# Kernel optimization log

Hardware: AMD Instinct MI355X
Metric: run time of the kernel (lower is better)

The kernel has to match this reference:

```python
import math
import jax, jax.numpy as jnp
import numpy as np

B, T, E = 16, 4096, 512


def setup_inputs() -> dict:
    key = jax.random.key(0)
    kq, kk, kv = jax.random.split(key, 3)
    Q = jax.random.normal(kq, (B, T, E), dtype=jnp.float32)
    K = jax.random.normal(kk, (B, T, E), dtype=jnp.float32)
    V = jax.random.normal(kv, (B, T, E), dtype=jnp.float32)
    return {"Q": Q, "K": K, "V": V}


def reference(Q, K, V):
    b, t, e = V.shape
    # --- FFT autocorrelation: replacement for QK^T ---
    qf = jnp.fft.rfft(Q, axis=1)
    kf = jnp.fft.rfft(K, axis=1)
    attn = jnp.fft.irfft(qf * jnp.conj(kf), n=t, axis=1)  # [B, T, E]

    # --- time-delay aggregation (autocorrelation_factor = 2) ---
    top_k = int(2 * math.log(t))                 # 16 for T=4096
    mean_corr = attn.mean(axis=-1)               # mean over heads(=1) & channel -> [B, T]
    global_mean = mean_corr.mean(axis=0)         # batch-shared delay scores [T]
    _, delays = jax.lax.top_k(global_mean, top_k)  # [top_k] int delays
    w = jax.nn.softmax(mean_corr[:, delays], axis=-1)  # per-batch weights [B, top_k]

    t_idx = jnp.arange(t)

    def body(acc, dw):
        d, wk = dw                               # scalar delay, [B] weights
        rolled = V[:, (t_idx + d) % t, :]        # roll(shifts=-d, dims=1) via modular gather
        return acc + rolled * wk[:, None, None], None

    out, _ = jax.lax.scan(body, jnp.zeros_like(V), (delays, w.T))
    return out
```

## Files before the change

### kernel.cpp

```cpp
#include <hip/hip_runtime.h>
#include <math.h>

#define TB 16
#define TT 4096
#define TE 512
#define NF 2049
#define TOPK 16

__device__ __forceinline__ int dr4(int u) {
  return ((u & 3) << 10) | (((u >> 2) & 3) << 8) | (((u >> 4) & 3) << 6) |
         (((u >> 6) & 3) << 4) | (((u >> 8) & 3) << 2) | ((u >> 10) & 3);
}
__device__ __forceinline__ int swz(int i) { return i ^ (i >> 4); }
__device__ __forceinline__ float2 cmul(float2 a, float2 b) {
  return make_float2(a.x * b.x - a.y * b.y, a.x * b.y + a.y * b.x);
}

extern "C" __global__ void __launch_bounds__(512)
k1_spec(const float* __restrict__ Qg, const float* __restrict__ Kg, float* __restrict__ S) {
  __shared__ float2 z[4][4096];
  __shared__ float2 tw[1024];
  const int tid = threadIdx.x;
  const int b   = blockIdx.x >> 4;
  const int grp = blockIdx.x & 15;

  for (int k = tid; k < 1024; k += 512) {
    float s, c;
    sincosf(-6.283185307179586f * (float)k / 4096.0f, &s, &c);
    tw[k] = make_float2(c, s);
  }

  float accr[5] = {0, 0, 0, 0, 0};
  float acci[5] = {0, 0, 0, 0, 0};
  const size_t base = (size_t)b * TT * TE;
  const int ch = tid >> 7;
  const int l  = tid & 127;

  for (int it = 0; it < 8; ++it) {
    const int e0 = grp * 32 + it * 4;
    __syncthreads();
    for (int j = 0; j < 8; ++j) {
      const int t = tid + 512 * j;
      const float4 q4 = *(const float4*)(Qg + base + (size_t)t * TE + e0);
      const float4 k4 = *(const float4*)(Kg + base + (size_t)t * TE + e0);
      const int p = swz(t);
      z[0][p] = make_float2(q4.x, k4.x);
      z[1][p] = make_float2(q4.y, k4.y);
      z[2][p] = make_float2(q4.z, k4.z);
      z[3][p] = make_float2(q4.w, k4.w);
    }
    __syncthreads();

    float2* zz = z[ch];
#pragma unroll
    for (int s = 0; s < 6; ++s) {
      const int M  = 4096 >> (2 * s);
      const int Qq = M >> 2;
      const int LQ = 10 - 2 * s;
      for (int q = 0; q < 8; ++q) {
        const int v    = l + 128 * q;
        const int blk  = v >> LQ;
        const int j    = v & (Qq - 1);
        const int bse  = blk * M + j;
        float2 a0 = zz[swz(bse)];
        float2 a1 = zz[swz(bse + Qq)];
        float2 a2 = zz[swz(bse + 2 * Qq)];
        float2 a3 = zz[swz(bse + 3 * Qq)];
        float2 t0 = {a0.x + a2.x, a0.y + a2.y};
        float2 t1 = {a0.x - a2.x, a0.y - a2.y};
        float2 t2 = {a1.x + a3.x, a1.y + a3.y};
        float2 t3 = {a1.x - a3.x, a1.y - a3.y};
        float2 u0 = {t0.x + t2.x, t0.y + t2.y};
        float2 u2 = {t0.x - t2.x, t0.y - t2.y};
        float2 u1 = {t1.x + t3.y, t1.y - t3.x};
        float2 u3 = {t1.x - t3.y, t1.y + t3.x};
        const float2 w1 = tw[j << (2 * s)];
        const float2 w2 = cmul(w1, w1);
        const float2 w3 = cmul(w1, w2);
        zz[swz(bse)]          = u0;
        zz[swz(bse + Qq)]     = cmul(u1, w1);
        zz[swz(bse + 2 * Qq)] = cmul(u2, w2);
        zz[swz(bse + 3 * Qq)] = cmul(u3, w3);
      }
      __syncthreads();
    }

#pragma unroll
    for (int r = 0; r < 5; ++r) {
      const int f = tid + 512 * r;
      if (f <= 2048) {
        const int u  = swz(dr4(f));
        const int u2 = swz(dr4((4096 - f) & 4095));
#pragma unroll
        for (int c = 0; c < 4; ++c) {
          const float2 Zf = z[c][u];
          float2 Zc = z[c][u2];
          Zc.y = -Zc.y;
          const float qx = 0.5f * (Zf.x + Zc.x), qy = 0.5f * (Zf.y + Zc.y);
          const float dx = Zf.x - Zc.x,          dy = Zf.y - Zc.y;
          const float kx = 0.5f * dy,            ky = -0.5f * dx;
          accr[r] += qx * kx + qy * ky;
          acci[r] += qy * kx - qx * ky;
        }
      }
    }
  }

#pragma unroll
  for (int r = 0; r < 5; ++r) {
    const int f = tid + 512 * r;
    if (f <= 2048) {
      atomicAdd(S + ((size_t)b * NF + f) * 2 + 0, accr[r]);
      atomicAdd(S + ((size_t)b * NF + f) * 2 + 1, acci[r]);
    }
  }
}

extern "C" __global__ void __launch_bounds__(512)
k2_irfft(const float* __restrict__ S, float* __restrict__ mc) {
  __shared__ float2 z[4096];
  __shared__ float2 tw[1024];
  const int tid = threadIdx.x;
  const int b   = blockIdx.x;
  for (int k = tid; k < 1024; k += 512) {
    float s, c;
    sincosf(6.283185307179586f * (float)k / 4096.0f, &s, &c);
    tw[k] = make_float2(c, s);
  }
  __syncthreads();
  const float scale = 1.0f / (4096.0f * 512.0f);
  for (int jj = 0; jj < 8; ++jj) {
    const int u = tid + 512 * jj;
    const int f = dr4(u);
    float2 v;
    if (f <= 2048) {
      v = make_float2(S[((size_t)b * NF + f) * 2], S[((size_t)b * NF + f) * 2 + 1]);
    } else {
      const int f2 = 4096 - f;
      v = make_float2(S[((size_t)b * NF + f2) * 2], -S[((size_t)b * NF + f2) * 2 + 1]);
    }
    z[swz(u)] = make_float2(v.x * scale, v.y * scale);
  }
  __syncthreads();
#pragma unroll
  for (int s = 5; s >= 0; --s) {
    const int M  = 4096 >> (2 * s);
    const int Qq = M >> 2;
    const int LQ = 10 - 2 * s;
    for (int q = 0; q < 2; ++q) {
      const int v   = tid + 512 * q;
      const int blk = v >> LQ;
      const int j   = v & (Qq - 1);
      const int bse = blk * M + j;
      float2 b0 = z[swz(bse)];
      float2 b1 = z[swz(bse + Qq)];
      float2 b2 = z[swz(bse + 2 * Qq)];
      float2 b3 = z[swz(bse + 3 * Qq)];
      const float2 w1 = tw[j << (2 * s)];
      const float2 w2 = cmul(w1, w1);
      const float2 w3 = cmul(w1, w2);
      b1 = cmul(b1, w1); b2 = cmul(b2, w2); b3 = cmul(b3, w3);
      float2 t0 = {b0.x + b2.x, b0.y + b2.y};
      float2 t1 = {b0.x - b2.x, b0.y - b2.y};
      float2 t2 = {b1.x + b3.x, b1.y + b3.y};
      float2 t3 = {b1.x - b3.x, b1.y - b3.y};
      z[swz(bse)]          = make_float2(t0.x + t2.x, t0.y + t2.y);
      z[swz(bse + Qq)]     = make_float2(t1.x - t3.y, t1.y + t3.x);
      z[swz(bse + 2 * Qq)] = make_float2(t0.x - t2.x, t0.y - t2.y);
      z[swz(bse + 3 * Qq)] = make_float2(t1.x + t3.y, t1.y - t3.x);
    }
    __syncthreads();
  }
  for (int jj = 0; jj < 8; ++jj) {
    const int t = tid + 512 * jj;
    mc[(size_t)b * TT + t] = z[swz(t)].x;
  }
}

extern "C" __global__ void __launch_bounds__(512)
k3_select(const float* __restrict__ mc, int* __restrict__ delays, float* __restrict__ wts) {
  __shared__ float gm[4096];
  __shared__ float red[512];
  __shared__ int   redi[512];
  __shared__ int   sel[TOPK];
  const int tid = threadIdx.x;
  for (int jj = 0; jj < 8; ++jj) {
    const int t = tid + 512 * jj;
    float ssum = 0.f;
    for (int b = 0; b < TB; ++b) ssum += mc[(size_t)b * TT + t];
    gm[t] = ssum;
  }
  __syncthreads();
  for (int k = 0; k < TOPK; ++k) {
    float best = -3.0e38f; int bi = 0x7fffffff;
    for (int jj = 0; jj < 8; ++jj) {
      const int t = tid + 512 * jj;
      const float v = gm[t];
      if (v > best || (v == best && t < bi)) { best = v; bi = t; }
    }
    red[tid] = best; redi[tid] = bi;
    __syncthreads();
    for (int s = 256; s > 0; s >>= 1) {
      if (tid < s) {
        if (red[tid + s] > red[tid] ||
            (red[tid + s] == red[tid] && redi[tid + s] < redi[tid])) {
          red[tid] = red[tid + s]; redi[tid] = redi[tid + s];
        }
      }
      __syncthreads();
    }
    if (tid == 0) { sel[k] = redi[0]; gm[redi[0]] = -3.0e38f; }
    __syncthreads();
  }
  if (tid < TOPK) delays[tid] = sel[tid];
  if (tid < TB * TOPK) {
    const int b = tid >> 4, k = tid & 15;
    const float v = mc[(size_t)b * TT + sel[k]];
    float m = v;
    for (int o = 8; o > 0; o >>= 1) m = fmaxf(m, __shfl_xor(m, o, 16));
    const float e = expf(v - m);
    float ssum = e;
    for (int o = 8; o > 0; o >>= 1) ssum += __shfl_xor(ssum, o, 16);
    wts[tid] = e / ssum;
  }
}

extern "C" __global__ void __launch_bounds__(256)
k4_out(const float* __restrict__ V, const int* __restrict__ delays,
       const float* __restrict__ wts, float* __restrict__ out) {
  __shared__ int   d_s[TOPK];
  __shared__ float w_s[TOPK];
  const int b  = blockIdx.x / (TT / 8);
  const int t0 = (blockIdx.x % (TT / 8)) * 8;
  const int tid = threadIdx.x;
  if (tid < TOPK) { d_s[tid] = delays[tid]; w_s[tid] = wts[b * TOPK + tid]; }
  __syncthreads();
  const int rowp = tid >> 7;
  const int e4   = tid & 127;
  const float* Vb = V   + (size_t)b * TT * TE;
  float*       Ob = out + (size_t)b * TT * TE;
  for (int p = 0; p < 4; ++p) {
    const int t = t0 + p * 2 + rowp;
    float4 acc = {0.f, 0.f, 0.f, 0.f};
#pragma unroll
    for (int k = 0; k < TOPK; ++k) {
      const int ts = (t + d_s[k]) & (TT - 1);
      const float4 v = *(const float4*)(Vb + (size_t)ts * TE + e4 * 4);
      const float w = w_s[k];
      acc.x += w * v.x; acc.y += w * v.y; acc.z += w * v.z; acc.w += w * v.w;
    }
    *(float4*)(Ob + (size_t)t * TE + e4 * 4) = acc;
  }
}

extern "C" void kernel_launch(void* const* d_in, const int* in_sizes, int n_in,
                              void* d_out, int out_size, void* d_ws, size_t ws_size,
                              hipStream_t stream) {
  const float* Q = (const float*)d_in[0];
  const float* K = (const float*)d_in[1];
  const float* V = (const float*)d_in[2];
  float* out = (float*)d_out;

  float* S      = (float*)d_ws;
  float* mc     = S + (size_t)TB * NF * 2;
  int*   delays = (int*)(mc + (size_t)TB * TT);
  float* wts    = (float*)(delays + TOPK);

  hipMemsetAsync(S, 0, (size_t)TB * NF * 2 * sizeof(float), stream);
  k1_spec<<<TB * 16, 512, 0, stream>>>(Q, K, S);
  k2_irfft<<<TB, 512, 0, stream>>>(S, mc);
  k3_select<<<1, 512, 0, stream>>>(mc, delays, wts);
  k4_out<<<TB * (TT / 8), 256, 0, stream>>>(V, delays, wts, out);
}
```

Baseline: 985.3 us.

## Pre-transpose Q and K to channel-major before FFT; shuffle-based top-k; XCD-aware output mapping

Adds a tiled transpose kernel that writes Q into the output buffer and K into workspace in [B,E,T] layout. The spectrum kernel can then load contiguous float4 runs along time instead of 16-byte strided reads across rows. The top-k selection switches to a wavefront shuffle reduction, and the output kernel remaps block IDs so each XCD handles contiguous batches. The cost is an extra full read/write pass over Q and K and a large workspace requirement, with a fallback to the old path when workspace is insufficient.

New measurement: 817.8 us. 1.2x faster.

```diff
diff --git a/kernel.cpp b/kernel.cpp
--- a/kernel.cpp
+++ b/kernel.cpp
@@ -16,8 +16,54 @@
   return make_float2(a.x * b.x - a.y * b.y, a.x * b.y + a.y * b.x);
 }
 
+extern "C" __global__ void __launch_bounds__(256)
+k0_transpose(const float* __restrict__ Q, const float* __restrict__ K,
+             float* __restrict__ Qt, float* __restrict__ Kt) {
+  __shared__ float tile[64][65];
+  const int tid = threadIdx.x;
+  const int bid = blockIdx.x;
+  const int b   = bid >> 9;
+  const int rem = bid & 511;
+  const int t0  = (rem >> 3) * 64;
+  const int e0  = (rem & 7) * 64;
+  const size_t inb  = (size_t)b * TT * TE;
+  const size_t outb = (size_t)b * TE * TT;
+  const int r0 = tid >> 4;
+  const int c0 = (tid & 15) * 4;
+
+#pragma unroll
+  for (int rr = 0; rr < 4; ++rr) {
+    const int r = r0 + 16 * rr;
+    const float4 v = *(const float4*)(Q + inb + (size_t)(t0 + r) * TE + e0 + c0);
+    tile[r][c0] = v.x; tile[r][c0 + 1] = v.y; tile[r][c0 + 2] = v.z; tile[r][c0 + 3] = v.w;
+  }
+  __syncthreads();
+#pragma unroll
+  for (int rr = 0; rr < 4; ++rr) {
+    const int er = r0 + 16 * rr;
+    float4 w;
+    w.x = tile[c0][er]; w.y = tile[c0 + 1][er]; w.z = tile[c0 + 2][er]; w.w = tile[c0 + 3][er];
+    *(float4*)(Qt + outb + (size_t)(e0 + er) * TT + t0 + c0) = w;
+  }
+  __syncthreads();
+#pragma unroll
+  for (int rr = 0; rr < 4; ++rr) {
+    const int r = r0 + 16 * rr;
+    const float4 v = *(const float4*)(K + inb + (size_t)(t0 + r) * TE + e0 + c0);
+    tile[r][c0] = v.x; tile[r][c0 + 1] = v.y; tile[r][c0 + 2] = v.z; tile[r][c0 + 3] = v.w;
+  }
+  __syncthreads();
+#pragma unroll
+  for (int rr = 0; rr < 4; ++rr) {
+    const int er = r0 + 16 * rr;
+    float4 w;
+    w.x = tile[c0][er]; w.y = tile[c0 + 1][er]; w.z = tile[c0 + 2][er]; w.w = tile[c0 + 3][er];
+    *(float4*)(Kt + outb + (size_t)(e0 + er) * TT + t0 + c0) = w;
+  }
+}
+
 extern "C" __global__ void __launch_bounds__(512)
-k1_spec(const float* __restrict__ Qg, const float* __restrict__ Kg, float* __restrict__ S) {
+k1_fast(const float* __restrict__ Qt, const float* __restrict__ Kt, float* __restrict__ S) {
   __shared__ float2 z[4][4096];
   __shared__ float2 tw[1024];
   const int tid = threadIdx.x;
@@ -32,22 +78,24 @@
 
   float accr[5] = {0, 0, 0, 0, 0};
   float acci[5] = {0, 0, 0, 0, 0};
-  const size_t base = (size_t)b * TT * TE;
   const int ch = tid >> 7;
   const int l  = tid & 127;
 
   for (int it = 0; it < 8; ++it) {
     const int e0 = grp * 32 + it * 4;
     __syncthreads();
+    const float* qrow = Qt + ((size_t)b * TE + e0 + ch) * TT;
+    const float* krow = Kt + ((size_t)b * TE + e0 + ch) * TT;
+#pragma unroll
     for (int j = 0; j < 8; ++j) {
-      const int t = tid + 512 * j;
-      const float4 q4 = *(const float4*)(Qg + base + (size_t)t * TE + e0);
-      const float4 k4 = *(const float4*)(Kg + base + (size_t)t * TE + e0);
-      const int p = swz(t);
-      z[0][p] = make_float2(q4.x, k4.x);
-      z[1][p] = make_float2(q4.y, k4.y);
-      z[2][p] = make_float2(q4.z, k4.z);
-      z[3][p] = make_float2(q4.w, k4.w);
+      const int t4 = l + 128 * j;
+      const float4 q4 = *(const float4*)(qrow + 4 * t4);
+      const float4 k4 = *(const float4*)(krow + 4 * t4);
+      const int t = 4 * t4;
+      z[ch][swz(t + 0)] = make_float2(q4.x, k4.x);
+      z[ch][swz(t + 1)] = make_float2(q4.y, k4.y);
+      z[ch][swz(t + 2)] = make_float2(q4.z, k4.z);
+      z[ch][swz(t + 3)] = make_float2(q4.w, k4.w);
     }
     __syncthreads();
 
@@ -117,6 +165,106 @@
 }
 
 extern "C" __global__ void __launch_bounds__(512)
+k1_spec(const float* __restrict__ Qg, const float* __restrict__ Kg, float* __restrict__ S) {
+  __shared__ float2 z[4][4096];
+  __shared__ float2 tw[1024];
+  const int tid = threadIdx.x;
+  const int b   = blockIdx.x >> 4;
+  const int grp = blockIdx.x & 15;
+
+  for (int k = tid; k < 1024; k += 512) {
+    float s, c;
+    sincosf(-6.283185307179586f * (float)k / 4096.0f, &s, &c);
+    tw[k] = make_float2(c, s);
+  }
+
+  float accr[5] = {0, 0, 0, 0, 0};
+  float acci[5] = {0, 0, 0, 0, 0};
+  const size_t base = (size_t)b * TT * TE;
+  const int ch = tid >> 7;
+  const int l  = tid & 127;
+
+  for (int it = 0; it < 8; ++it) {
+    const int e0 = grp * 32 + it * 4;
+    __syncthreads();
+    for (int j = 0; j < 8; ++j) {
+      const int t = tid + 512 * j;
+      const float4 q4 = *(const float4*)(Qg + base + (size_t)t * TE + e0);
+      const float4 k4 = *(const float4*)(Kg + base + (size_t)t * TE + e0);
+      const int p = swz(t);
+      z[0][p] = make_float2(q4.x, k4.x);
+      z[1][p] = make_float2(q4.y, k4.y);
+      z[2][p] = make_float2(q4.z, k4.z);
+      z[3][p] = make_float2(q4.w, k4.w);
+    }
+    __syncthreads();
+
+    float2* zz = z[ch];
+#pragma unroll
+    for (int s = 0; s < 6; ++s) {
+      const int M  = 4096 >> (2 * s);
+      const int Qq = M >> 2;
+      const int LQ = 10 - 2 * s;
+      for (int q = 0; q < 8; ++q) {
+        const int v    = l + 128 * q;
+        const int blk  = v >> LQ;
+        const int j    = v & (Qq - 1);
+        const int bse  = blk * M + j;
+        float2 a0 = zz[swz(bse)];
+        float2 a1 = zz[swz(bse + Qq)];
+        float2 a2 = zz[swz(bse + 2 * Qq)];
+        float2 a3 = zz[swz(bse + 3 * Qq)];
+        float2 t0 = {a0.x + a2.x, a0.y + a2.y};
+        float2 t1 = {a0.x - a2.x, a0.y - a2.y};
+        float2 t2 = {a1.x + a3.x, a1.y + a3.y};
+        float2 t3 = {a1.x - a3.x, a1.y - a3.y};
+        float2 u0 = {t0.x + t2.x, t0.y + t2.y};
+        float2 u2 = {t0.x - t2.x, t0.y - t2.y};
+        float2 u1 = {t1.x + t3.y, t1.y - t3.x};
+        float2 u3 = {t1.x - t3.y, t1.y + t3.x};
+        const float2 w1 = tw[j << (2 * s)];
+        const float2 w2 = cmul(w1, w1);
+        const float2 w3 = cmul(w1, w2);
+        zz[swz(bse)]          = u0;
+        zz[swz(bse + Qq)]     = cmul(u1, w1);
+        zz[swz(bse + 2 * Qq)] = cmul(u2, w2);
+        zz[swz(bse + 3 * Qq)] = cmul(u3, w3);
+      }
+      __syncthreads();
+    }
+
+#pragma unroll
+    for (int r = 0; r < 5; ++r) {
+      const int f = tid + 512 * r;
+      if (f <= 2048) {
+        const int u  = swz(dr4(f));
+        const int u2 = swz(dr4((4096 - f) & 4095));
+#pragma unroll
+        for (int c = 0; c < 4; ++c) {
+          const float2 Zf = z[c][u];
+          float2 Zc = z[c][u2];
+          Zc.y = -Zc.y;
+          const float qx = 0.5f * (Zf.x + Zc.x), qy = 0.5f * (Zf.y + Zc.y);
+          const float dx = Zf.x - Zc.x,          dy = Zf.y - Zc.y;
+          const float kx = 0.5f * dy,            ky = -0.5f * dx;
+          accr[r] += qx * kx + qy * ky;
+          acci[r] += qy * kx - qx * ky;
+        }
+      }
+    }
+  }
+
+#pragma unroll
+  for (int r = 0; r < 5; ++r) {
+    const int f = tid + 512 * r;
+    if (f <= 2048) {
+      atomicAdd(S + ((size_t)b * NF + f) * 2 + 0, accr[r]);
+      atomicAdd(S + ((size_t)b * NF + f) * 2 + 1, acci[r]);
+    }
+  }
+}
+
+extern "C" __global__ void __launch_bounds__(512)
 k2_irfft(const float* __restrict__ S, float* __restrict__ mc) {
   __shared__ float2 z[4096];
   __shared__ float2 tw[1024];
@@ -180,10 +328,12 @@
 extern "C" __global__ void __launch_bounds__(512)
 k3_select(const float* __restrict__ mc, int* __restrict__ delays, float* __restrict__ wts) {
   __shared__ float gm[4096];
-  __shared__ float red[512];
-  __shared__ int   redi[512];
+  __shared__ float redv[8];
+  __shared__ int   redi[8];
   __shared__ int   sel[TOPK];
-  const int tid = threadIdx.x;
+  const int tid  = threadIdx.x;
+  const int lane = tid & 63;
+  const int wv   = tid >> 6;
   for (int jj = 0; jj < 8; ++jj) {
     const int t = tid + 512 * jj;
     float ssum = 0.f;
@@ -193,23 +343,26 @@
   __syncthreads();
   for (int k = 0; k < TOPK; ++k) {
     float best = -3.0e38f; int bi = 0x7fffffff;
+#pragma unroll
     for (int jj = 0; jj < 8; ++jj) {
       const int t = tid + 512 * jj;
       const float v = gm[t];
       if (v > best || (v == best && t < bi)) { best = v; bi = t; }
     }
-    red[tid] = best; redi[tid] = bi;
-    __syncthreads();
-    for (int s = 256; s > 0; s >>= 1) {
-      if (tid < s) {
-        if (red[tid + s] > red[tid] ||
-            (red[tid + s] == red[tid] && redi[tid + s] < redi[tid])) {
-          red[tid] = red[tid + s]; redi[tid] = redi[tid + s];
-        }
-      }
-      __syncthreads();
-    }
-    if (tid == 0) { sel[k] = redi[0]; gm[redi[0]] = -3.0e38f; }
+#pragma unroll
+    for (int o = 32; o > 0; o >>= 1) {
+      const float ov = __shfl_xor(best, o);
+      const int   oi = __shfl_xor(bi, o);
+      if (ov > best || (ov == best && oi < bi)) { best = ov; bi = oi; }
+    }
+    if (lane == 0) { redv[wv] = best; redi[wv] = bi; }
+    __syncthreads();
+    if (tid == 0) {
+      float bb = redv[0]; int ii = redi[0];
+      for (int w = 1; w < 8; ++w)
+        if (redv[w] > bb || (redv[w] == bb && redi[w] < ii)) { bb = redv[w]; ii = redi[w]; }
+      sel[k] = ii; gm[ii] = -3.0e38f;
+    }
     __syncthreads();
   }
   if (tid < TOPK) delays[tid] = sel[tid];
@@ -230,8 +383,11 @@
        const float* __restrict__ wts, float* __restrict__ out) {
   __shared__ int   d_s[TOPK];
   __shared__ float w_s[TOPK];
-  const int b  = blockIdx.x / (TT / 8);
-  const int t0 = (blockIdx.x % (TT / 8)) * 8;
+  const int bid = blockIdx.x;
+  const int xcd = bid & 7;
+  const int loc = bid >> 3;
+  const int b   = 2 * xcd + (loc >> 9);
+  const int t0  = (loc & 511) * 8;
   const int tid = threadIdx.x;
   if (tid < TOPK) { d_s[tid] = delays[tid]; w_s[tid] = wts[b * TOPK + tid]; }
   __syncthreads();
@@ -261,14 +417,34 @@
   const float* V = (const float*)d_in[2];
   float* out = (float*)d_out;
 
-  float* S      = (float*)d_ws;
-  float* mc     = S + (size_t)TB * NF * 2;
-  int*   delays = (int*)(mc + (size_t)TB * TT);
-  float* wts    = (float*)(delays + TOPK);
-
-  hipMemsetAsync(S, 0, (size_t)TB * NF * 2 * sizeof(float), stream);
-  k1_spec<<<TB * 16, 512, 0, stream>>>(Q, K, S);
-  k2_irfft<<<TB, 512, 0, stream>>>(S, mc);
-  k3_select<<<1, 512, 0, stream>>>(mc, delays, wts);
-  k4_out<<<TB * (TT / 8), 256, 0, stream>>>(V, delays, wts, out);
-}
+  const size_t KT_FLOATS = (size_t)TB * TE * TT;
+  const size_t AUX_FLOATS = (size_t)TB * NF * 2 + (size_t)TB * TT + 16 + TB * TOPK;
+  const size_t NEED = (KT_FLOATS + AUX_FLOATS) * sizeof(float);
+
+  if (ws_size >= NEED) {
+    float* Qt     = out;
+    float* Kt     = (float*)d_ws;
+    float* S      = Kt + KT_FLOATS;
+    float* mc     = S + (size_t)TB * NF * 2;
+    int*   delays = (int*)(mc + (size_t)TB * TT);
+    float* wts    = (float*)(delays + TOPK);
+
+    hipMemsetAsync(S, 0, (size_t)TB * NF * 2 * sizeof(float), stream);
+    k0_transpose<<<TB * 512, 256, 0, stream>>>(Q, K, Qt, Kt);
+    k1_fast<<<TB * 16, 512, 0, stream>>>(Qt, Kt, S);
+    k2_irfft<<<TB, 512, 0, stream>>>(S, mc);
+    k3_select<<<1, 512, 0, stream>>>(mc, delays, wts);
+    k4_out<<<TB * (TT / 8), 256, 0, stream>>>(V, delays, wts, out);
+  } else {
+    float* S      = (float*)d_ws;
+    float* mc     = S + (size_t)TB * NF * 2;
+    int*   delays = (int*)(mc + (size_t)TB * TT);
+    float* wts    = (float*)(delays + TOPK);
+
+    hipMemsetAsync(S, 0, (size_t)TB * NF * 2 * sizeof(float), stream);
+    k1_spec<<<TB * 16, 512, 0, stream>>>(Q, K, S);
+    k2_irfft<<<TB, 512, 0, stream>>>(S, mc);
+    k3_select<<<1, 512, 0, stream>>>(mc, delays, wts);
+    k4_out<<<TB * (TT / 8), 256, 0, stream>>>(V, delays, wts, out);
+  }
+}
```
